# Performance work log

Hardware: AMD Instinct MI355X
Metric: run time of the kernel (lower is better)

## Reference

```python
import jax, jax.numpy as jnp
import numpy as np


def setup_inputs() -> dict:
    key = jax.random.key(0)
    ks = jax.random.split(key, 6)
    B, T, D, H = 2, 2048, 1024, 16
    dk = D // H
    s = 0.02
    return {
        "x": jax.random.normal(ks[0], (B, T, D), dtype=jnp.float32),
        "Wq": jax.random.normal(ks[1], (H, dk, dk), dtype=jnp.float32) * s,
        "Wk": jax.random.normal(ks[2], (H, dk, dk), dtype=jnp.float32) * s,
        "Wv": jax.random.normal(ks[3], (H, dk, dk), dtype=jnp.float32) * s,
        "Wp": jax.random.normal(ks[4], (D, D), dtype=jnp.float32) * s,
        "bp": jnp.zeros((D,), dtype=jnp.float32),
    }


def reference(x, Wq, Wk, Wv, Wp, bp):
    B, T, D = x.shape
    H, dk, _ = Wq.shape
    # split into heads: [B, H, T, dk]
    xh = x.reshape(B, T, H, dk).transpose(0, 2, 1, 3)
    # per-head torch Linear (y = x @ W^T), all heads at once
    q = jnp.einsum('bhtd,hkd->bhtk', xh, Wq)
    k = jnp.einsum('bhtd,hkd->bhtk', xh, Wk)
    v = jnp.einsum('bhtd,hkd->bhtk', xh, Wv)
    scale = 1.0 / jnp.sqrt(jnp.float32(dk))  # original divides by sqrt(C) with C == d_k
    scores = jnp.einsum('bhqd,bhkd->bhqk', q, k) * scale
    causal = jnp.tril(jnp.ones((T, T), dtype=bool))
    scores = jnp.where(causal[None, None], scores, -jnp.inf)
    attn = jax.nn.softmax(scores, axis=-1)
    out = jnp.einsum('bhqk,bhkd->bhqd', attn, v)  # [B,H,T,dk]
    out = out.transpose(0, 2, 1, 3).reshape(B, T, D)  # concat heads
    return out @ Wp.T + bp
```

## Files before the change

### kernel.cpp

```cpp
#include <hip/hip_runtime.h>
#include <math.h>

#define B_ 2
#define T_ 2048
#define D_ 1024
#define H_ 16
#define DK 64
#define BH_ (B_*H_)

typedef __attribute__((ext_vector_type(8))) short short8;
typedef __attribute__((ext_vector_type(4))) float fragC;

#define MFMA32(A,B,C) __builtin_amdgcn_mfma_f32_16x16x32_bf16((A),(B),(C),0,0,0)

__device__ __forceinline__ unsigned short f2bf(float x) {
    union { float f; unsigned u; } c; c.f = x;
    unsigned r = c.u + 0x7fff + ((c.u >> 16) & 1);
    return (unsigned short)(r >> 16);
}

__device__ __forceinline__ unsigned pack2bf(float a, float b) {
    return (unsigned)f2bf(a) | ((unsigned)f2bf(b) << 16);
}

__device__ __forceinline__ unsigned permpack(float a, float b) {
    union { float f; unsigned u; } ca, cb; ca.f = a; cb.f = b;
    return __builtin_amdgcn_perm(cb.u, ca.u, 0x07060302);
}

__device__ __forceinline__ short8 packbf8(float4 a, float4 b) {
    union { short8 v; unsigned u[4]; } r;
    r.u[0] = pack2bf(a.x, a.y); r.u[1] = pack2bf(a.z, a.w);
    r.u[2] = pack2bf(b.x, b.y); r.u[3] = pack2bf(b.z, b.w);
    return r.v;
}

__device__ __forceinline__ void gload_lds16(const void* g, void* l) {
    __builtin_amdgcn_global_load_lds(
        (const __attribute__((address_space(1))) unsigned int*)g,
        (__attribute__((address_space(3))) unsigned int*)l, 16, 0, 0);
}

__global__ __launch_bounds__(256) void qkv_kernel(
    const float* __restrict__ x,
    const float* __restrict__ Wq, const float* __restrict__ Wk,
    const float* __restrict__ Wv, const float* __restrict__ Wp,
    unsigned short* __restrict__ Wb,
    unsigned short* __restrict__ q, unsigned short* __restrict__ k,
    unsigned short* __restrict__ vt)
{
    __shared__ unsigned short Wl[3*64*64];

    const int bh = blockIdx.x;
    const int b  = bh >> 4, h = bh & 15;
    const int t0 = blockIdx.y * 128;
    const int tid = threadIdx.x;
    const int wave = tid >> 6, lane = tid & 63;
    const int n = lane & 15, quad = lane >> 4;

    {
        const int L = bh + (blockIdx.y << 5);
        const float* src = Wp + (size_t)L*2048 + tid*8;
        float4 a = *(const float4*)src;
        float4 b2 = *(const float4*)(src + 4);
        *(uint4*)(Wb + (size_t)L*2048 + tid*8) =
            make_uint4(pack2bf(a.x, a.y), pack2bf(a.z, a.w),
                       pack2bf(b2.x, b2.y), pack2bf(b2.z, b2.w));
    }

    #pragma unroll
    for (int mat = 0; mat < 3; ++mat) {
        const float* ws = ((mat == 0) ? Wq : (mat == 1) ? Wk : Wv)
                          + (size_t)h * 4096;
        #pragma unroll
        for (int j = 0; j < 2; ++j) {
            const int e = (j*256 + tid) * 8;
            float4 a = *(const float4*)&ws[e];
            float4 b2 = *(const float4*)&ws[e + 4];
            *(uint4*)&Wl[mat*4096 + e] =
                make_uint4(pack2bf(a.x, a.y), pack2bf(a.z, a.w),
                           pack2bf(b2.x, b2.y), pack2bf(b2.z, b2.w));
        }
    }

    const int tw = t0 + wave*32;
    short8 xf[2][2];
    #pragma unroll
    for (int rt = 0; rt < 2; ++rt) {
        const float* xr = &x[((size_t)b*T_ + tw + rt*16 + n)*D_ + h*DK];
        float4 a0 = *(const float4*)&xr[quad*8];
        float4 a1 = *(const float4*)&xr[quad*8 + 4];
        xf[rt][0] = packbf8(a0, a1);
        float4 b0 = *(const float4*)&xr[32 + quad*8];
        float4 b1 = *(const float4*)&xr[32 + quad*8 + 4];
        xf[rt][1] = packbf8(b0, b1);
    }
    __syncthreads();

    const float qsc = 0.125f * 1.44269504088896340736f;
    const int tb0 = blockIdx.y*8 + wave*2;
    #pragma unroll
    for (int mat = 0; mat < 3; ++mat) {
        const int wbase = mat * 4096;
        #pragma unroll
        for (int ct = 0; ct < 4; ++ct) {
            short8 wf0 = *(const short8*)&Wl[wbase + (ct*16 + n)*64 + quad*8];
            short8 wf1 = *(const short8*)&Wl[wbase + (ct*16 + n)*64 + 32 + quad*8];
            if (mat < 2) {
                #pragma unroll
                for (int rt = 0; rt < 2; ++rt) {
                    fragC z = {0.f,0.f,0.f,0.f};
                    z = MFMA32(wf0, xf[rt][0], z);
                    z = MFMA32(wf1, xf[rt][1], z);
                    if (mat == 0) {
                        z[0] *= qsc; z[1] *= qsc; z[2] *= qsc; z[3] *= qsc;
                    }
                    unsigned short* dstg = (mat == 0) ? q : k;
                    unsigned short* dp = &dstg[((size_t)bh*128 + tb0 + rt)*1024
                                               + (ct*2 + (quad>>1))*128 + n*8 + (quad&1)*4];
                    *(uint2*)dp = make_uint2(pack2bf(z[0], z[1]), pack2bf(z[2], z[3]));
                }
            } else {
                uint4 pv4;
                {
                    fragC z = {0.f,0.f,0.f,0.f};
                    z = MFMA32(xf[0][0], wf0, z);
                    z = MFMA32(xf[0][1], wf1, z);
                    pv4.x = pack2bf(z[0], z[1]); pv4.y = pack2bf(z[2], z[3]);
                }
                {
                    fragC z = {0.f,0.f,0.f,0.f};
                    z = MFMA32(xf[1][0], wf0, z);
                    z = MFMA32(xf[1][1], wf1, z);
                    pv4.z = pack2bf(z[0], z[1]); pv4.w = pack2bf(z[2], z[3]);
                }
                const int ktv = tw >> 6, pv = (tw >> 5) & 1;
                unsigned short* dp = &vt[(size_t)bh*131072 + ktv*4096
                                         + ct*1024 + pv*512 + lane*8];
                *(uint4*)dp = pv4;
            }
        }
    }
}

__global__ __launch_bounds__(256, 2) void attn_kernel(
    const unsigned short* __restrict__ q, const unsigned short* __restrict__ k,
    const unsigned short* __restrict__ vt, unsigned short* __restrict__ aout)
{
    __shared__ fragC Os[4][4][4][64];
    __shared__ float Ls[4][4][16];

    const int id = blockIdx.x;
    const int xc = id & 7, p = id >> 3;
    const int jj = p & 3, s = p >> 2, g = s & 7, r = s >> 3;
    const int bh = xc*4 + jj;
    const int qt = (r == 0) ? 31 - g : (r == 1) ? g : (r == 2) ? 23 - g : 8 + g;

    const int b   = bh >> 4, h = bh & 15;
    const int tid = threadIdx.x;
    const int w = tid >> 6, lane = tid & 63;
    const int n = lane & 15, quad = lane >> 4;

    short8 qf[4][2];
    #pragma unroll
    for (int qc = 0; qc < 4; ++qc) {
        const unsigned short* qb = &q[((size_t)bh*128 + qt*4 + qc)*1024 + n*8];
        qf[qc][0] = *(const short8*)&qb[quad*128];
        qf[qc][1] = *(const short8*)&qb[(4 + quad)*128];
    }

    fragC o[4][4];
    #pragma unroll
    for (int qc = 0; qc < 4; ++qc)
        #pragma unroll
        for (int dt = 0; dt < 4; ++dt) o[qc][dt] = (fragC){0.f,0.f,0.f,0.f};
    fragC l[4];
    #pragma unroll
    for (int qc = 0; qc < 4; ++qc) l[qc] = (fragC){0.f,0.f,0.f,0.f};

    short8 ones8;
    #pragma unroll
    for (int jo = 0; jo < 8; ++jo) ones8[jo] = (short)0x3F80;

    const unsigned short* kg = &k[(size_t)bh*131072 + lane*8];
    const unsigned short* vg = &vt[(size_t)bh*131072 + lane*8];
    const int nt = qt + 1;

    short8 kf[4][2];
    short8 vv[4][2];

    int t = w;
    if (t < nt) {
        #pragma unroll
        for (int ct = 0; ct < 4; ++ct) {
            kf[ct][0] = *(const short8*)&kg[t*4096 + ct*1024];
            kf[ct][1] = *(const short8*)&kg[t*4096 + ct*1024 + 512];
        }
    }

    for (; t < nt; t += 4) {
        #pragma unroll
        for (int dt = 0; dt < 4; ++dt) {
            vv[dt][0] = *(const short8*)&vg[t*4096 + dt*1024];
            vv[dt][1] = *(const short8*)&vg[t*4096 + dt*1024 + 512];
        }

        const bool diag = (t == qt);
        #pragma unroll
        for (int qc = 0; qc < 4; ++qc) {
            union { short8 v; unsigned u[4]; } pb[2];
            #pragma unroll
            for (int cp = 0; cp < 2; ++cp) {
                fragC c[2];
                __builtin_amdgcn_s_setprio(1);
                #pragma unroll
                for (int c2 = 0; c2 < 2; ++c2) {
                    const int ct = cp*2 + c2;
                    fragC z = {0.f,0.f,0.f,0.f};
                    z = MFMA32(kf[ct][0], qf[qc][0], z);
                    z = MFMA32(kf[ct][1], qf[qc][1], z);
                    c[c2] = z;
                }
                __builtin_amdgcn_s_setprio(0);
                #pragma unroll
                for (int c2 = 0; c2 < 2; ++c2) {
                    const int ct = cp*2 + c2;
                    float p0 = exp2f(c[c2][0]), p1 = exp2f(c[c2][1]);
                    float p2 = exp2f(c[c2][2]), p3 = exp2f(c[c2][3]);
                    if (diag) {
                        const int lim = (qc*16 + n) - (ct*16 + quad*4);
                        if (0 > lim) p0 = 0.f;
                        if (1 > lim) p1 = 0.f;
                        if (2 > lim) p2 = 0.f;
                        if (3 > lim) p3 = 0.f;
                    }
                    pb[cp].u[c2*2]     = permpack(p0, p1);
                    pb[cp].u[c2*2 + 1] = permpack(p2, p3);
                }
            }

            if (qc == 3 && t + 4 < nt) {
                #pragma unroll
                for (int ct = 0; ct < 4; ++ct) {
                    kf[ct][0] = *(const short8*)&kg[(t+4)*4096 + ct*1024];
                    kf[ct][1] = *(const short8*)&kg[(t+4)*4096 + ct*1024 + 512];
                }
            }

            __builtin_amdgcn_s_setprio(1);
            #pragma unroll
            for (int pv = 0; pv < 2; ++pv) {
                l[qc] = MFMA32(ones8, pb[pv].v, l[qc]);
                #pragma unroll
                for (int dt = 0; dt < 4; ++dt)
                    o[qc][dt] = MFMA32(vv[dt][pv], pb[pv].v, o[qc][dt]);
            }
            __builtin_amdgcn_s_setprio(0);
        }
    }

    #pragma unroll
    for (int qc = 0; qc < 4; ++qc) {
        #pragma unroll
        for (int dt = 0; dt < 4; ++dt)
            Os[w][qc][dt][lane] = o[qc][dt];
        if (quad == 0) Ls[w][qc][n] = l[qc][0];
    }
    __syncthreads();

    const float lsum = Ls[0][w][n] + Ls[1][w][n] + Ls[2][w][n] + Ls[3][w][n];
    const float inv = 1.0f / lsum;
    const int q0 = qt*64 + w*16;
    unsigned short* dp = &aout[((size_t)b*T_ + q0 + n)*D_ + h*DK + quad*4];
    #pragma unroll
    for (int dt = 0; dt < 4; ++dt) {
        fragC sum = Os[0][w][dt][lane] + Os[1][w][dt][lane]
                  + Os[2][w][dt][lane] + Os[3][w][dt][lane];
        *(uint2*)(dp + dt*16) =
            make_uint2(pack2bf(sum[0]*inv, sum[1]*inv),
                       pack2bf(sum[2]*inv, sum[3]*inv));
    }
}

__global__ __launch_bounds__(256) void proj_kernel(
    const unsigned short* __restrict__ A, const unsigned short* __restrict__ Wb,
    const float* __restrict__ bp, float* __restrict__ out)
{
    __shared__ unsigned short As[2][128*64];
    __shared__ unsigned short Bs[2][128*64];

    const int id = blockIdx.x;
    const int m0 = (((id & 7) << 2) + ((id >> 3) >> 3)) << 7;
    const int n0 = (((id >> 3) & 7)) << 7;
    const int tid = threadIdx.x;
    const int wave = tid >> 6, lane = tid & 63;
    const int wm = wave & 1, wn = wave >> 1;
    const int n = lane & 15, quad = lane >> 4;

    const int srow = wave*32 + (lane >> 3);
    const int scol = (lane & 7) * 8;
    const unsigned short* ag = &A [(size_t)(m0 + srow)*1024 + scol];
    const unsigned short* bg = &Wb[(size_t)(n0 + srow)*1024 + scol];

    fragC acc[4][4];
    #pragma unroll
    for (int i = 0; i < 4; ++i)
        #pragma unroll
        for (int j = 0; j < 4; ++j) acc[i][j] = (fragC){0.f,0.f,0.f,0.f};

    auto stage = [&](int bu, int kt) {
        unsigned short* al = &As[bu][srow*64 + scol];
        unsigned short* bl = &Bs[bu][srow*64 + scol];
        #pragma unroll
        for (int i = 0; i < 4; ++i) {
            gload_lds16(ag + (size_t)i*8192 + kt*64, al + i*512);
            gload_lds16(bg + (size_t)i*8192 + kt*64, bl + i*512);
        }
    };

    stage(0, 0);
    for (int kt = 0; kt < 16; ++kt) {
        __syncthreads();
        if (kt < 15) stage((kt + 1) & 1, kt + 1);
        const unsigned short* Ab = As[kt & 1];
        const unsigned short* Bb = Bs[kt & 1];
        #pragma unroll
        for (int kk = 0; kk < 2; ++kk) {
            short8 af[4], bf[4];
            #pragma unroll
            for (int i = 0; i < 4; ++i)
                af[i] = *(const short8*)&Ab[(wm*64 + i*16 + n)*64 + kk*32 + quad*8];
            #pragma unroll
            for (int j = 0; j < 4; ++j)
                bf[j] = *(const short8*)&Bb[(wn*64 + j*16 + n)*64 + kk*32 + quad*8];
            #pragma unroll
            for (int i = 0; i < 4; ++i)
                #pragma unroll
                for (int j = 0; j < 4; ++j)
                    acc[i][j] = MFMA32(af[i], bf[j], acc[i][j]);
        }
    }

    #pragma unroll
    for (int i = 0; i < 4; ++i) {
        #pragma unroll
        for (int r = 0; r < 4; ++r) {
            const int m = m0 + wm*64 + i*16 + quad*4 + r;
            #pragma unroll
            for (int j = 0; j < 4; ++j) {
                const int col = n0 + wn*64 + j*16 + n;
                out[(size_t)m*1024 + col] = acc[i][j][r] + bp[col];
            }
        }
    }
}

extern "C" void kernel_launch(void* const* d_in, const int* in_sizes, int n_in,
                              void* d_out, int out_size, void* d_ws, size_t ws_size,
                              hipStream_t stream)
{
    const float* x  = (const float*)d_in[0];
    const float* Wq = (const float*)d_in[1];
    const float* Wk = (const float*)d_in[2];
    const float* Wv = (const float*)d_in[3];
    const float* Wp = (const float*)d_in[4];
    const float* bp = (const float*)d_in[5];
    float* out = (float*)d_out;

    const size_t per = (size_t)BH_ * T_ * DK;
    unsigned short* qws   = (unsigned short*)d_ws;
    unsigned short* kws   = qws + per;
    unsigned short* vtws  = kws + per;
    unsigned short* aws   = vtws + per;
    unsigned short* wbws  = aws + per;

    qkv_kernel<<<dim3(BH_, T_/128), 256, 0, stream>>>(x, Wq, Wk, Wv, Wp, wbws,
                                                      qws, kws, vtws);
    attn_kernel<<<dim3(1024), 256, 0, stream>>>(qws, kws, vtws, aws);
    proj_kernel<<<dim3(256), 256, 0, stream>>>(aws, wbws, bp, out);
}
```

Baseline: 139.3 us.

## Restructure attention inner loop scheduling and retile projection GEMM to 64x128

In the attention kernel, all QK^T MFMAs for pairs of query chunks are issued before the exp/pack work, the P·V MFMAs are grouped after all softmax values are computed, and the V tile loads move to the end of each iteration as a prefetch for the next tile. The projection GEMM moves from 128x128 to 64x128 tiles, launches 512 blocks instead of 256, uses an XCD-aware block mapping and sets launch bounds for 3 blocks per CU. The aim is more MFMA/VALU overlap in attention and better CU occupancy in the small GEMM. The cost is higher register pressure from the larger score and packed-P arrays, and less data reuse per projection tile.

After: 136.6 us. About the same (-1.9%).

```diff
diff --git a/kernel.cpp b/kernel.cpp
--- a/kernel.cpp
+++ b/kernel.cpp
@@ -196,37 +196,49 @@
             kf[ct][0] = *(const short8*)&kg[t*4096 + ct*1024];
             kf[ct][1] = *(const short8*)&kg[t*4096 + ct*1024 + 512];
         }
-    }
-
-    for (; t < nt; t += 4) {
         #pragma unroll
         for (int dt = 0; dt < 4; ++dt) {
             vv[dt][0] = *(const short8*)&vg[t*4096 + dt*1024];
             vv[dt][1] = *(const short8*)&vg[t*4096 + dt*1024 + 512];
         }
-
+    }
+
+    for (; t < nt; t += 4) {
         const bool diag = (t == qt);
-        #pragma unroll
-        for (int qc = 0; qc < 4; ++qc) {
-            union { short8 v; unsigned u[4]; } pb[2];
-            #pragma unroll
-            for (int cp = 0; cp < 2; ++cp) {
-                fragC c[2];
-                __builtin_amdgcn_s_setprio(1);
-                #pragma unroll
-                for (int c2 = 0; c2 < 2; ++c2) {
-                    const int ct = cp*2 + c2;
+        unsigned pu[4][8];
+
+        #pragma unroll
+        for (int qp = 0; qp < 2; ++qp) {
+            fragC c[2][4];
+            __builtin_amdgcn_s_setprio(1);
+            #pragma unroll
+            for (int q2 = 0; q2 < 2; ++q2) {
+                const int qc = qp*2 + q2;
+                #pragma unroll
+                for (int ct = 0; ct < 4; ++ct) {
                     fragC z = {0.f,0.f,0.f,0.f};
                     z = MFMA32(kf[ct][0], qf[qc][0], z);
                     z = MFMA32(kf[ct][1], qf[qc][1], z);
-                    c[c2] = z;
-                }
-                __builtin_amdgcn_s_setprio(0);
-                #pragma unroll
-                for (int c2 = 0; c2 < 2; ++c2) {
-                    const int ct = cp*2 + c2;
-                    float p0 = exp2f(c[c2][0]), p1 = exp2f(c[c2][1]);
-                    float p2 = exp2f(c[c2][2]), p3 = exp2f(c[c2][3]);
+                    c[q2][ct] = z;
+                }
+            }
+            __builtin_amdgcn_s_setprio(0);
+
+            if (qp == 1 && t + 4 < nt) {
+                #pragma unroll
+                for (int ct = 0; ct < 4; ++ct) {
+                    kf[ct][0] = *(const short8*)&kg[(t+4)*4096 + ct*1024];
+                    kf[ct][1] = *(const short8*)&kg[(t+4)*4096 + ct*1024 + 512];
+                }
+            }
+
+            #pragma unroll
+            for (int q2 = 0; q2 < 2; ++q2) {
+                const int qc = qp*2 + q2;
+                #pragma unroll
+                for (int ct = 0; ct < 4; ++ct) {
+                    float p0 = exp2f(c[q2][ct][0]), p1 = exp2f(c[q2][ct][1]);
+                    float p2 = exp2f(c[q2][ct][2]), p3 = exp2f(c[q2][ct][3]);
                     if (diag) {
                         const int lim = (qc*16 + n) - (ct*16 + quad*4);
                         if (0 > lim) p0 = 0.f;
@@ -234,28 +246,34 @@
                         if (2 > lim) p2 = 0.f;
                         if (3 > lim) p3 = 0.f;
                     }
-                    pb[cp].u[c2*2]     = permpack(p0, p1);
-                    pb[cp].u[c2*2 + 1] = permpack(p2, p3);
-                }
-            }
-
-            if (qc == 3 && t + 4 < nt) {
-                #pragma unroll
-                for (int ct = 0; ct < 4; ++ct) {
-                    kf[ct][0] = *(const short8*)&kg[(t+4)*4096 + ct*1024];
-                    kf[ct][1] = *(const short8*)&kg[(t+4)*4096 + ct*1024 + 512];
-                }
-            }
-
-            __builtin_amdgcn_s_setprio(1);
+                    pu[qc][(ct>>1)*4 + (ct&1)*2]     = permpack(p0, p1);
+                    pu[qc][(ct>>1)*4 + (ct&1)*2 + 1] = permpack(p2, p3);
+                }
+            }
+        }
+
+        __builtin_amdgcn_s_setprio(1);
+        #pragma unroll
+        for (int qc = 0; qc < 4; ++qc) {
             #pragma unroll
             for (int pv = 0; pv < 2; ++pv) {
-                l[qc] = MFMA32(ones8, pb[pv].v, l[qc]);
+                union { unsigned u[4]; short8 v; } pk;
+                pk.u[0] = pu[qc][pv*4];     pk.u[1] = pu[qc][pv*4 + 1];
+                pk.u[2] = pu[qc][pv*4 + 2]; pk.u[3] = pu[qc][pv*4 + 3];
+                l[qc] = MFMA32(ones8, pk.v, l[qc]);
                 #pragma unroll
                 for (int dt = 0; dt < 4; ++dt)
-                    o[qc][dt] = MFMA32(vv[dt][pv], pb[pv].v, o[qc][dt]);
-            }
-            __builtin_amdgcn_s_setprio(0);
+                    o[qc][dt] = MFMA32(vv[dt][pv], pk.v, o[qc][dt]);
+            }
+        }
+        __builtin_amdgcn_s_setprio(0);
+
+        if (t + 4 < nt) {
+            #pragma unroll
+            for (int dt = 0; dt < 4; ++dt) {
+                vv[dt][0] = *(const short8*)&vg[(t+4)*4096 + dt*1024];
+                vv[dt][1] = *(const short8*)&vg[(t+4)*4096 + dt*1024 + 512];
+            }
         }
     }
 
@@ -282,40 +300,39 @@
     }
 }
 
-__global__ __launch_bounds__(256) void proj_kernel(
+__global__ __launch_bounds__(256, 3) void proj_kernel(
     const unsigned short* __restrict__ A, const unsigned short* __restrict__ Wb,
     const float* __restrict__ bp, float* __restrict__ out)
 {
-    __shared__ unsigned short As[2][128*64];
+    __shared__ unsigned short As[2][64*64];
     __shared__ unsigned short Bs[2][128*64];
 
     const int id = blockIdx.x;
-    const int m0 = (((id & 7) << 2) + ((id >> 3) >> 3)) << 7;
-    const int n0 = (((id >> 3) & 7)) << 7;
+    const int xcd = id & 7, idx = id >> 3;
+    const int m0 = (xcd*8 + (idx & 7)) * 64;
+    const int n0 = (idx >> 3) * 128;
     const int tid = threadIdx.x;
     const int wave = tid >> 6, lane = tid & 63;
     const int wm = wave & 1, wn = wave >> 1;
     const int n = lane & 15, quad = lane >> 4;
 
-    const int srow = wave*32 + (lane >> 3);
-    const int scol = (lane & 7) * 8;
-    const unsigned short* ag = &A [(size_t)(m0 + srow)*1024 + scol];
-    const unsigned short* bg = &Wb[(size_t)(n0 + srow)*1024 + scol];
-
-    fragC acc[4][4];
-    #pragma unroll
-    for (int i = 0; i < 4; ++i)
+    const int arow = tid >> 3, acol = (tid & 7) * 8;
+    const unsigned short* ag = &A [(size_t)(m0 + arow)*1024 + acol];
+    const unsigned short* bg = &Wb[(size_t)(n0 + arow)*1024 + acol];
+
+    fragC acc[2][4];
+    #pragma unroll
+    for (int i = 0; i < 2; ++i)
         #pragma unroll
         for (int j = 0; j < 4; ++j) acc[i][j] = (fragC){0.f,0.f,0.f,0.f};
 
     auto stage = [&](int bu, int kt) {
-        unsigned short* al = &As[bu][srow*64 + scol];
-        unsigned short* bl = &Bs[bu][srow*64 + scol];
-        #pragma unroll
-        for (int i = 0; i < 4; ++i) {
-            gload_lds16(ag + (size_t)i*8192 + kt*64, al + i*512);
-            gload_lds16(bg + (size_t)i*8192 + kt*64, bl + i*512);
-        }
+        #pragma unroll
+        for (int i2 = 0; i2 < 2; ++i2)
+            gload_lds16(ag + (size_t)i2*32*1024 + kt*64, &As[bu][i2*2048 + tid*8]);
+        #pragma unroll
+        for (int j2 = 0; j2 < 4; ++j2)
+            gload_lds16(bg + (size_t)j2*32*1024 + kt*64, &Bs[bu][j2*2048 + tid*8]);
     };
 
     stage(0, 0);
@@ -326,15 +343,15 @@
         const unsigned short* Bb = Bs[kt & 1];
         #pragma unroll
         for (int kk = 0; kk < 2; ++kk) {
-            short8 af[4], bf[4];
-            #pragma unroll
-            for (int i = 0; i < 4; ++i)
-                af[i] = *(const short8*)&Ab[(wm*64 + i*16 + n)*64 + kk*32 + quad*8];
+            short8 af[2], bf[4];
+            #pragma unroll
+            for (int i = 0; i < 2; ++i)
+                af[i] = *(const short8*)&Ab[(wm*32 + i*16 + n)*64 + kk*32 + quad*8];
             #pragma unroll
             for (int j = 0; j < 4; ++j)
                 bf[j] = *(const short8*)&Bb[(wn*64 + j*16 + n)*64 + kk*32 + quad*8];
             #pragma unroll
-            for (int i = 0; i < 4; ++i)
+            for (int i = 0; i < 2; ++i)
                 #pragma unroll
                 for (int j = 0; j < 4; ++j)
                     acc[i][j] = MFMA32(af[i], bf[j], acc[i][j]);
@@ -342,10 +359,10 @@
     }
 
     #pragma unroll
-    for (int i = 0; i < 4; ++i) {
+    for (int i = 0; i < 2; ++i) {
         #pragma unroll
         for (int r = 0; r < 4; ++r) {
-            const int m = m0 + wm*64 + i*16 + quad*4 + r;
+            const int m = m0 + wm*32 + i*16 + quad*4 + r;
             #pragma unroll
             for (int j = 0; j < 4; ++j) {
                 const int col = n0 + wn*64 + j*16 + n;
@@ -377,5 +394,5 @@
     qkv_kernel<<<dim3(BH_, T_/128), 256, 0, stream>>>(x, Wq, Wk, Wv, Wp, wbws,
                                                       qws, kws, vtws);
     attn_kernel<<<dim3(1024), 256, 0, stream>>>(qws, kws, vtws, aws);
-    proj_kernel<<<dim3(256), 256, 0, stream>>>(aws, wbws, bp, out);
-}
+    proj_kernel<<<dim3(512), 256, 0, stream>>>(aws, wbws, bp, out);
+}
```
